# Performance work log

Measured on AMD Instinct MI355X. Metric: run time of the kernel, lower is better.

The kernel has to match this reference:

```python
import jax, jax.numpy as jnp
import numpy as np

B, N, E = 4, 2048, 512
H, DK, DV = 8, 64, 64
QKV_OUT = H * (2 * DK + DV)  # 1536


def setup_inputs() -> dict:
    key = jax.random.key(0)
    ks = jax.random.split(key, 5)
    s_in = 1.0 / np.sqrt(E)
    s_o = 1.0 / np.sqrt(H * DV)
    x = jax.random.normal(ks[0], (B, N, E), dtype=jnp.float32)
    W_qkv = jax.random.uniform(ks[1], (E, QKV_OUT), jnp.float32, -s_in, s_in)
    b_qkv = jax.random.uniform(ks[2], (QKV_OUT,), jnp.float32, -s_in, s_in)
    W_o = jax.random.uniform(ks[3], (H * DV, E), jnp.float32, -s_o, s_o)
    b_o = jax.random.uniform(ks[4], (E,), jnp.float32, -s_o, s_o)
    return {"x": x, "W_qkv": W_qkv, "b_qkv": b_qkv, "W_o": W_o, "b_o": b_o}


def reference(x, W_qkv, b_qkv, W_o, b_o):
    scale = DK ** (-0.5)
    qkv = x @ W_qkv + b_qkv                      # [B, N, H*(2dk+dv)]
    # Faithful to torch: raw view (B, H, N, 2dk+dv), NOT a head-split transpose.
    qkv = qkv.reshape(B, H, N, 2 * DK + DV)
    q = qkv[..., :DK]
    k = qkv[..., DK:2 * DK]
    v = qkv[..., 2 * DK:]
    # Faithful bug: qk /= scale with scale = dk^-0.5 -> multiply by sqrt(dk).
    qk = jnp.einsum('bhnd,bhmd->bhnm', q, k) / scale   # [B, H, N, N]
    attn = jax.nn.softmax(qk, axis=-1)
    y = jnp.einsum('bhnm,bhmd->bhnd', attn, v)         # [B, H, N, dv]
    y = y.reshape(B, N, H * DV)
    return y @ W_o + b_o
```

## Files before the change

### kernel.cpp

```cpp
#include <hip/hip_runtime.h>
#include <hip/hip_bf16.h>
#include <math.h>


typedef __attribute__((ext_vector_type(8))) short bf16x8;
typedef __attribute__((ext_vector_type(4))) float f32x4;

#define MFMA16(a, b, c) __builtin_amdgcn_mfma_f32_16x16x32_bf16((a), (b), (c), 0, 0, 0)

__device__ __forceinline__ ushort f2bf_rne(float f) {
  union { float f; unsigned u; } v; v.f = f;
  return (ushort)((v.u + 0x7fffu + ((v.u >> 16) & 1u)) >> 16);
}
__device__ __forceinline__ float bf2f(ushort h) {
  union { float f; unsigned u; } v; v.u = ((unsigned)h) << 16; return v.f;
}
__device__ __forceinline__ void split2(float f, ushort& hi, ushort& lo) {
  union { float f; unsigned u; } v; v.f = f;
  hi = (ushort)(v.u >> 16);
  union { float f; unsigned u; } r; r.f = f - bf2f(hi);
  lo = (ushort)(r.u >> 16);
}

typedef __attribute__((address_space(3))) unsigned int lds_uint;
typedef const __attribute__((address_space(1))) unsigned int glob_uint;
__device__ __forceinline__ void gl_lds16(const ushort* g, short* l) {
  __builtin_amdgcn_global_load_lds((glob_uint*)g, (lds_uint*)l, 16, 0, 0);
}

template <bool ROOMY>
__global__ __launch_bounds__(256) void cvt_k(const float* __restrict__ wqkv,
                                             const float* __restrict__ wo,
                                             const float* __restrict__ x,
                                             ushort* __restrict__ wT_hi,
                                             ushort* __restrict__ wT_lo,
                                             ushort* __restrict__ woT,
                                             ushort* __restrict__ xh,
                                             ushort* __restrict__ xl)
{
  const int gid = blockIdx.x * 256 + threadIdx.x;
  if (gid < 786432) {
    const int c   = gid / 49152;
    const int rem = gid - c * 49152;
    const int n   = rem >> 5;
    const int k   = c * 32 + (rem & 31);
    ushort hi, lo; split2(wqkv[(size_t)k * 1536 + n], hi, lo);
    wT_hi[gid] = hi; wT_lo[gid] = lo;
  } else if (gid < 1048576) {
    const int g = gid - 786432;
    const int n = g >> 9, k = g & 511;
    woT[g] = f2bf_rne(wo[(size_t)k * 512 + n]);
  } else if (ROOMY) {
    const int g = gid - 1048576;
    float4 v = ((const float4*)x)[g];
    ushort4 hh, ll;
    split2(v.x, hh.x, ll.x); split2(v.y, hh.y, ll.y);
    split2(v.z, hh.z, ll.z); split2(v.w, hh.w, ll.w);
    ((ushort4*)xh)[g] = hh;
    ((ushort4*)xl)[g] = ll;
  }
}

template <bool PRECVT>
__global__ __launch_bounds__(256) void qkv_gemm_k(
    const float* __restrict__ x,
    const ushort* __restrict__ xh, const ushort* __restrict__ xl,
    const ushort* __restrict__ wT_hi, const ushort* __restrict__ wT_lo,
    const float* __restrict__ bqkv,
    ushort* __restrict__ q_hi, ushort* __restrict__ q_lo,
    ushort* __restrict__ k_hi, ushort* __restrict__ k_lo,
    ushort* __restrict__ v_nat)
{
  const int i = blockIdx.x, j = i >> 3;
  const int tmb = (i & 7) * 8 + (j & 7);
  const int tn  = j >> 3;
  const int tid = threadIdx.x, lane = tid & 63, w = tid >> 6;
  const int col16 = lane & 15, quad = lane >> 4;
  const int wr = w >> 1, wc = w & 1;

  __shared__ short sbuf[16384];

  const int wl   = w * 1024 + lane * 8;
  const int ldsw = w * 1024;
  const ushort* shp = wT_hi + (size_t)tn * 4096 + wl;
  const ushort* slp = wT_lo + (size_t)tn * 4096 + wl;

  const float*  axf[4];
  const ushort *axh[4], *axl[4];
#pragma unroll
  for (int rt = 0; rt < 4; ++rt) {
    const size_t rowoff = (size_t)(tmb * 128 + wr * 64 + rt * 16 + col16) * 512 + quad * 8;
    axf[rt] = x  + rowoff;
    axh[rt] = xh + rowoff;
    axl[rt] = xl + rowoff;
  }

  f32x4 acc[4][4];
#pragma unroll
  for (int rt = 0; rt < 4; ++rt)
#pragma unroll
    for (int ct = 0; ct < 4; ++ct) acc[rt][ct] = (f32x4){0.f, 0.f, 0.f, 0.f};

  gl_lds16(shp,       sbuf + ldsw);
  gl_lds16(shp + 512, sbuf + ldsw + 512);
  gl_lds16(slp,       sbuf + 8192 + ldsw);
  gl_lds16(slp + 512, sbuf + 8192 + ldsw + 512);
  __syncthreads();

  int buf = 0;
#pragma unroll
  for (int c = 0; c < 16; ++c) {
    if (c < 15) {
      const size_t co = (size_t)(c + 1) * 49152;
      const int nb = (buf ^ 1) * 4096;
      gl_lds16(shp + co,       sbuf + nb + ldsw);
      gl_lds16(shp + co + 512, sbuf + nb + ldsw + 512);
      gl_lds16(slp + co,       sbuf + 8192 + nb + ldsw);
      gl_lds16(slp + co + 512, sbuf + 8192 + nb + ldsw + 512);
    }
    const int k0 = c * 32;
    const short* bhb = sbuf + buf * 4096;
    const short* blb = sbuf + 8192 + buf * 4096;

    bf16x8 bh[4], bl[4];
#pragma unroll
    for (int ct = 0; ct < 4; ++ct) {
      const int roff = (wc * 64 + ct * 16 + col16) * 32 + quad * 8;
      bh[ct] = *(const bf16x8*)(bhb + roff);
      bl[ct] = *(const bf16x8*)(blb + roff);
    }
#pragma unroll
    for (int rt = 0; rt < 4; ++rt) {
      bf16x8 a_hi, a_lo;
      if constexpr (PRECVT) {
        a_hi = *(const bf16x8*)(axh[rt] + k0);
        a_lo = *(const bf16x8*)(axl[rt] + k0);
      } else {
        float4 xa = *(const float4*)(axf[rt] + k0);
        float4 xb = *(const float4*)(axf[rt] + k0 + 4);
#pragma unroll
        for (int jj = 0; jj < 4; ++jj) {
          ushort h, l;
          split2(((const float*)&xa)[jj], h, l);
          ((short*)&a_hi)[jj] = (short)h; ((short*)&a_lo)[jj] = (short)l;
          split2(((const float*)&xb)[jj], h, l);
          ((short*)&a_hi)[4 + jj] = (short)h; ((short*)&a_lo)[4 + jj] = (short)l;
        }
      }
#pragma unroll
      for (int ct = 0; ct < 4; ++ct) {
        acc[rt][ct] = MFMA16(a_hi, bh[ct], acc[rt][ct]);
        acc[rt][ct] = MFMA16(a_hi, bl[ct], acc[rt][ct]);
        acc[rt][ct] = MFMA16(a_lo, bh[ct], acc[rt][ct]);
      }
    }
    __syncthreads();
    buf ^= 1;
  }

  short* eph = sbuf + w * 2304;
  short* epl = eph + 1152;
  const int g0   = tn * 128 + wc * 64;
  const int sect = (g0 % 192) >> 6;
  const int s    = g0 / 192;
  float bv[4];
#pragma unroll
  for (int ct = 0; ct < 4; ++ct) bv[ct] = bqkv[g0 + ct * 16 + col16];

#pragma unroll
  for (int rt = 0; rt < 4; ++rt) {
#pragma unroll
    for (int ct = 0; ct < 4; ++ct) {
#pragma unroll
      for (int r = 0; r < 4; ++r) {
        const float val = acc[rt][ct][r] + bv[ct];
        const int o = (quad * 4 + r) * 72 + ct * 16 + col16;
        if (sect == 2) {
          eph[o] = (short)f2bf_rne(val);
        } else {
          ushort h, l; split2(val, h, l);
          eph[o] = (short)h; epl[o] = (short)l;
        }
      }
    }
#pragma unroll
    for (int p = 0; p < 2; ++p) {
      const int row = p * 8 + (lane >> 3);
      const int dsg = (lane & 7) * 8;
      const int grow = tmb * 128 + wr * 64 + rt * 16 + row;
      const int bhh = grow >> 8, a = grow & 255;
      const size_t idx = ((size_t)bhh * 2048 + 8 * a + s) * 64 + dsg;
      uint4 hv = *(const uint4*)(eph + row * 72 + dsg);
      if (sect == 0) {
        *(uint4*)(q_hi + idx) = hv;
        uint4 lv = *(const uint4*)(epl + row * 72 + dsg);
        *(uint4*)(q_lo + idx) = lv;
      } else if (sect == 1) {
        *(uint4*)(k_hi + idx) = hv;
        uint4 lv = *(const uint4*)(epl + row * 72 + dsg);
        *(uint4*)(k_lo + idx) = lv;
      } else {
        *(uint4*)(v_nat + idx) = hv;
      }
    }
  }
}

__global__ __launch_bounds__(256) void vtrans_k(const ushort* __restrict__ v_nat,
                                                ushort* __restrict__ vT)
{
  const int t  = blockIdx.x & 7;
  const int bh = blockIdx.x >> 3;
  const int tid = threadIdx.x;
  const int nl = tid & 63;
  const int dg = tid >> 6;
  const size_t base = (size_t)bh * 2048 * 64;
#pragma unroll
  for (int p = 0; p < 2; ++p) {
    const int dseg = dg + p * 4;
#pragma unroll
    for (int nb = 0; nb < 4; ++nb) {
      const int n = t * 256 + nb * 64 + nl;
      uint4 vv = *(const uint4*)(v_nat + base + (size_t)n * 64 + dseg * 8);
      const ushort* pv = (const ushort*)&vv;
#pragma unroll
      for (int j = 0; j < 8; ++j)
        vT[base + (size_t)(dseg * 8 + j) * 2048 + n] = pv[j];
    }
  }
}

__global__ __launch_bounds__(512, 4) void attn_k(
    const ushort* __restrict__ q_hi, const ushort* __restrict__ q_lo,
    const ushort* __restrict__ k_hi, const ushort* __restrict__ k_lo,
    const ushort* __restrict__ vT, ushort* __restrict__ y)
{
  const int i  = blockIdx.x;
  const int bh = (i & 7) * 4 + (i >> 7);
  const int qt = (i >> 3) & 15;
  const int tid = threadIdx.x, lane = tid & 63, w = tid >> 6;
  const int col16 = lane & 15, quad = lane >> 4;
  const int n7 = col16 & 7;

  __shared__ short sbuf[32768];

  const size_t base = (size_t)bh * 2048 * 64;
  const int qw = qt * 128 + w * 16;

  const ushort* khs = k_hi + base;
  const ushort* kls = k_lo + base;
  const ushort* vts = vT  + base;

  const int lrow = lane >> 3;
  const int lx8  = ((lane & 7) ^ lrow) * 8;

  bf16x8 qh[2], ql[2];
#pragma unroll
  for (int ks = 0; ks < 2; ++ks) {
    const size_t off = base + (size_t)(qw + col16) * 64 + ks * 32 + quad * 8;
    qh[ks] = *(const bf16x8*)(q_hi + off);
    ql[ks] = *(const bf16x8*)(q_lo + off);
  }

  f32x4 oacc[4];
#pragma unroll
  for (int ct = 0; ct < 4; ++ct) oacc[ct] = (f32x4){0.f, 0.f, 0.f, 0.f};
  float lsum = 0.f;

  const float S2 = 11.541560327111707f;

  short* wp0 = sbuf + 24576 + w * 1024;

#define STAGE_CHUNK(cnext, nb)                                                \
  {                                                                           \
    _Pragma("unroll")                                                         \
    for (int ii = 0; ii < 3; ++ii) {                                          \
      const int ins = w * 3 + ii;                                             \
      const int plane = ins >> 3, sub = ins & 7;                              \
      short* dst = sbuf + ((nb) * 3 + plane) * 4096 + sub * 512;              \
      const ushort* src;                                                      \
      if (plane == 2)                                                         \
        src = vts + (size_t)(sub * 8 + lrow) * 2048 + (cnext) * 64 + lx8;     \
      else                                                                    \
        src = (plane ? kls : khs) + (cnext) * 4096 + sub * 512 + lrow * 64 + lx8; \
      gl_lds16(src, dst);                                                     \
    }                                                                         \
  }

#define ATTN_CHUNK(C, BUF)                                                    \
  {                                                                           \
    if ((C) < 31) STAGE_CHUNK((C) + 1, (BUF) ^ 1);                            \
    const short* kb = sbuf + ((BUF) * 3) * 4096;                              \
    const short* lb = kb + 4096;                                              \
    const short* vb = kb + 8192;                                              \
    f32x4 sacc[4];                                                            \
    _Pragma("unroll")                                                         \
    for (int ct = 0; ct < 4; ++ct) sacc[ct] = (f32x4){0.f, 0.f, 0.f, 0.f};    \
    __builtin_amdgcn_s_setprio(1);                                            \
    _Pragma("unroll")                                                         \
    for (int ks = 0; ks < 2; ++ks) {                                          \
      _Pragma("unroll")                                                       \
      for (int ct = 0; ct < 4; ++ct) {                                        \
        const int off = (ct * 16 + col16) * 64 + (((ks * 4 + quad) ^ n7) << 3); \
        bf16x8 khf = *(const bf16x8*)(kb + off);                              \
        bf16x8 klf = *(const bf16x8*)(lb + off);                              \
        sacc[ct] = MFMA16(khf, qh[ks], sacc[ct]);                             \
        sacc[ct] = MFMA16(klf, qh[ks], sacc[ct]);                             \
        sacc[ct] = MFMA16(khf, ql[ks], sacc[ct]);                             \
      }                                                                       \
    }                                                                         \
    __builtin_amdgcn_s_setprio(0);                                            \
    _Pragma("unroll")                                                         \
    for (int ct = 0; ct < 4; ++ct) {                                          \
      union { float f; unsigned u; } p0, p1, p2, p3;                          \
      p0.f = __builtin_amdgcn_exp2f(fmaf(sacc[ct][0], S2, -128.0f));          \
      p1.f = __builtin_amdgcn_exp2f(fmaf(sacc[ct][1], S2, -128.0f));          \
      p2.f = __builtin_amdgcn_exp2f(fmaf(sacc[ct][2], S2, -128.0f));          \
      p3.f = __builtin_amdgcn_exp2f(fmaf(sacc[ct][3], S2, -128.0f));          \
      lsum += (p0.f + p1.f) + (p2.f + p3.f);                                  \
      const unsigned lo = (p0.u >> 16) | (p1.u & 0xffff0000u);                \
      const unsigned hi = (p2.u >> 16) | (p3.u & 0xffff0000u);                \
      const int g8 = (ct * 2 + (quad >> 1)) ^ n7;                             \
      uint2 pk; pk.x = lo; pk.y = hi;                                         \
      *(uint2*)(wp0 + col16 * 64 + (g8 << 3) + ((quad & 1) << 2)) = pk;       \
    }                                                                         \
    __builtin_amdgcn_s_setprio(1);                                            \
    _Pragma("unroll")                                                         \
    for (int ks = 0; ks < 2; ++ks) {                                          \
      bf16x8 ap = *(const bf16x8*)(wp0 + col16 * 64 +                         \
                                   (((ks * 4 + quad) ^ n7) << 3));            \
      _Pragma("unroll")                                                       \
      for (int ct = 0; ct < 4; ++ct) {                                        \
        const int voff = (ct * 16 + col16) * 64 + (((ks * 4 + quad) ^ n7) << 3); \
        bf16x8 vv = *(const bf16x8*)(vb + voff);                              \
        oacc[ct] = MFMA16(ap, vv, oacc[ct]);                                  \
      }                                                                       \
    }                                                                         \
    __builtin_amdgcn_s_setprio(0);                                            \
    __syncthreads();                                                          \
  }

  STAGE_CHUNK(0, 0);
  __syncthreads();

  for (int c = 0; c < 32; c += 2) {
    ATTN_CHUNK(c, 0);
    ATTN_CHUNK(c + 1, 1);
  }

  lsum += __shfl_xor(lsum, 16, 64);
  lsum += __shfl_xor(lsum, 32, 64);
#pragma unroll
  for (int r = 0; r < 4; ++r) {
    const float inv = 1.f / __shfl(lsum, quad * 4 + r, 64);
    const int n = qw + quad * 4 + r;
    const size_t orow = ((size_t)bh * 256 + (n >> 3)) * 512 + (n & 7) * 64;
#pragma unroll
    for (int ct = 0; ct < 4; ++ct)
      y[orow + ct * 16 + col16] = f2bf_rne(oacc[ct][r] * inv);
  }
#undef ATTN_CHUNK
#undef STAGE_CHUNK
}

__global__ __launch_bounds__(256) void out_gemm_k(
    const ushort* __restrict__ y, const ushort* __restrict__ woT,
    const float* __restrict__ bo, float* __restrict__ out)
{
  const int i = blockIdx.x, j = i >> 3;
  const int tmb = (i & 7) * 32 + (j & 31);
  const int tn  = j >> 5;
  const int tid = threadIdx.x, lane = tid & 63, w = tid >> 6;
  const int col16 = lane & 15, quad = lane >> 4;
  const int wr = w >> 1, wc = w & 1;

  __shared__ short b_lds[2][128][40];

  const int sn = tid >> 1, sk = (tid & 1) * 16;
  const ushort* bsrc = woT + (size_t)(tn * 128 + sn) * 512 + sk;

  const ushort* ay = y + (size_t)(tmb * 32 + wr * 16 + col16) * 512 + quad * 8;

  f32x4 acc[4];
#pragma unroll
  for (int ct = 0; ct < 4; ++ct) acc[ct] = (f32x4){0.f, 0.f, 0.f, 0.f};

  uint4 rb0 = *(const uint4*)(bsrc);
  uint4 rb1 = *(const uint4*)(bsrc + 8);
  *(uint4*)(&b_lds[0][sn][sk])     = rb0;
  *(uint4*)(&b_lds[0][sn][sk + 8]) = rb1;

  for (int c = 0; c < 16; ++c) {
    __syncthreads();
    if (c < 15) {
      const int k0 = (c + 1) * 32;
      rb0 = *(const uint4*)(bsrc + k0);
      rb1 = *(const uint4*)(bsrc + k0 + 8);
    }
    const int b = c & 1, k0 = c * 32;
    bf16x8 af = *(const bf16x8*)(ay + k0);
#pragma unroll
    for (int ct = 0; ct < 4; ++ct) {
      bf16x8 bfr = *(const bf16x8*)(&b_lds[b][wc * 64 + ct * 16 + col16][quad * 8]);
      acc[ct] = MFMA16(af, bfr, acc[ct]);
    }
    if (c < 15) {
      const int nb = b ^ 1;
      *(uint4*)(&b_lds[nb][sn][sk])     = rb0;
      *(uint4*)(&b_lds[nb][sn][sk + 8]) = rb1;
    }
  }
#pragma unroll
  for (int ct = 0; ct < 4; ++ct) {
    const int col = tn * 128 + wc * 64 + ct * 16 + col16;
    const float bval = bo[col];
#pragma unroll
    for (int r = 0; r < 4; ++r) {
      const int row = tmb * 32 + wr * 16 + quad * 4 + r;
      out[(size_t)row * 512 + col] = acc[ct][r] + bval;
    }
  }
}

extern "C" void kernel_launch(void* const* d_in, const int* in_sizes, int n_in,
                              void* d_out, int out_size, void* d_ws, size_t ws_size,
                              hipStream_t stream)
{
  const float* x    = (const float*)d_in[0];
  const float* Wqkv = (const float*)d_in[1];
  const float* bqkv = (const float*)d_in[2];
  const float* Wo   = (const float*)d_in[3];
  const float* bo   = (const float*)d_in[4];
  float* out = (float*)d_out;

  ushort* wT_hi = (ushort*)d_ws;
  ushort* wT_lo = wT_hi + 786432;
  ushort* woT   = wT_lo + 786432;
  ushort* q_hi  = woT   + 262144;
  ushort* q_lo  = q_hi  + 4194304;
  ushort* k_hi  = q_lo  + 4194304;
  ushort* k_lo  = k_hi  + 4194304;
  ushort* v_nat = k_lo  + 4194304;
  ushort* tail  = v_nat + 4194304;

  const bool roomy = ws_size >= 62390272ULL;
  ushort *xh, *xl, *vT, *y;
  if (roomy) {
    xh = tail; xl = tail + 4194304;
    vT = xh;   y  = xl;
  } else {
    xh = xl = nullptr;
    vT = tail; y = v_nat;
  }

  if (roomy) {
    cvt_k<true><<<8192, 256, 0, stream>>>(Wqkv, Wo, x, wT_hi, wT_lo, woT, xh, xl);
    qkv_gemm_k<true><<<768, 256, 0, stream>>>(x, xh, xl, wT_hi, wT_lo, bqkv,
                                              q_hi, q_lo, k_hi, k_lo, v_nat);
  } else {
    cvt_k<false><<<4096, 256, 0, stream>>>(Wqkv, Wo, x, wT_hi, wT_lo, woT,
                                           nullptr, nullptr);
    qkv_gemm_k<false><<<768, 256, 0, stream>>>(x, nullptr, nullptr, wT_hi, wT_lo,
                                               bqkv, q_hi, q_lo, k_hi, k_lo, v_nat);
  }
  vtrans_k<<<256, 256, 0, stream>>>(v_nat, vT);
  attn_k<<<512, 512, 0, stream>>>(q_hi, q_lo, k_hi, k_lo, vT, y);
  out_gemm_k<<<1024, 256, 0, stream>>>(y, woT, bo, out);
}
```

Before: 223.7 us.

## Chunk-major Wo layout and direct global-to-LDS staging in output GEMM

The converted W_o is stored chunk-major, in 32-wide k-chunks of contiguous [n][32] tiles, matching the layout already used for W_qkv. The output GEMM then streams each B chunk straight into LDS with gl_lds16 (global-to-LDS loads) instead of loading into registers and writing to a padded LDS array. This removes the register round trip and the extra LDS stores and saves VGPRs. In exchange the LDS tile is unpadded, which may cause bank conflicts on the fragment reads, and it relies on the helper's ordering being correct with one barrier per iteration.

Measured after the change: 222.6 us. About the same (-0.5%).

```diff
diff --git a/kernel.cpp b/kernel.cpp
--- a/kernel.cpp
+++ b/kernel.cpp
@@ -47,8 +47,11 @@
     ushort hi, lo; split2(wqkv[(size_t)k * 1536 + n], hi, lo);
     wT_hi[gid] = hi; wT_lo[gid] = lo;
   } else if (gid < 1048576) {
-    const int g = gid - 786432;
-    const int n = g >> 9, k = g & 511;
+    const int g   = gid - 786432;
+    const int c   = g / 16384;
+    const int rem = g - c * 16384;
+    const int n   = rem >> 5;
+    const int k   = c * 32 + (rem & 31);
     woT[g] = f2bf_rne(wo[(size_t)k * 512 + n]);
   } else if (ROOMY) {
     const int g = gid - 1048576;
@@ -374,10 +377,9 @@
   const int col16 = lane & 15, quad = lane >> 4;
   const int wr = w >> 1, wc = w & 1;
 
-  __shared__ short b_lds[2][128][40];
-
-  const int sn = tid >> 1, sk = (tid & 1) * 16;
-  const ushort* bsrc = woT + (size_t)(tn * 128 + sn) * 512 + sk;
+  __shared__ short sb[8192];
+
+  const ushort* bch = woT + (size_t)tn * 4096 + lane * 8;
 
   const ushort* ay = y + (size_t)(tmb * 32 + wr * 16 + col16) * 512 + quad * 8;
 
@@ -385,31 +387,37 @@
 #pragma unroll
   for (int ct = 0; ct < 4; ++ct) acc[ct] = (f32x4){0.f, 0.f, 0.f, 0.f};
 
-  uint4 rb0 = *(const uint4*)(bsrc);
-  uint4 rb1 = *(const uint4*)(bsrc + 8);
-  *(uint4*)(&b_lds[0][sn][sk])     = rb0;
-  *(uint4*)(&b_lds[0][sn][sk + 8]) = rb1;
-
+#define OSTAGE(cn, nb)                                                        \
+  {                                                                           \
+    _Pragma("unroll")                                                         \
+    for (int ii = 0; ii < 2; ++ii) {                                          \
+      const int ins = w * 2 + ii;                                             \
+      gl_lds16(bch + (size_t)(cn) * 16384 + ins * 512,                        \
+               sb + (nb) * 4096 + ins * 512);                                 \
+    }                                                                         \
+  }
+
+  OSTAGE(0, 0);
+  __syncthreads();
+
+  int buf = 0;
+#pragma unroll
   for (int c = 0; c < 16; ++c) {
+    if (c < 15) OSTAGE(c + 1, buf ^ 1);
+    const int k0 = c * 32;
+    const short* bb = sb + buf * 4096;
+    bf16x8 af = *(const bf16x8*)(ay + k0);
+#pragma unroll
+    for (int ct = 0; ct < 4; ++ct) {
+      const int roff = (wc * 64 + ct * 16 + col16) * 32 + quad * 8;
+      bf16x8 bfr = *(const bf16x8*)(bb + roff);
+      acc[ct] = MFMA16(af, bfr, acc[ct]);
+    }
     __syncthreads();
-    if (c < 15) {
-      const int k0 = (c + 1) * 32;
-      rb0 = *(const uint4*)(bsrc + k0);
-      rb1 = *(const uint4*)(bsrc + k0 + 8);
-    }
-    const int b = c & 1, k0 = c * 32;
-    bf16x8 af = *(const bf16x8*)(ay + k0);
-#pragma unroll
-    for (int ct = 0; ct < 4; ++ct) {
-      bf16x8 bfr = *(const bf16x8*)(&b_lds[b][wc * 64 + ct * 16 + col16][quad * 8]);
-      acc[ct] = MFMA16(af, bfr, acc[ct]);
-    }
-    if (c < 15) {
-      const int nb = b ^ 1;
-      *(uint4*)(&b_lds[nb][sn][sk])     = rb0;
-      *(uint4*)(&b_lds[nb][sn][sk + 8]) = rb1;
-    }
-  }
+    buf ^= 1;
+  }
+#undef OSTAGE
+
 #pragma unroll
   for (int ct = 0; ct < 4; ++ct) {
     const int col = tn * 128 + wc * 64 + ct * 16 + col16;
```
